# Kernel tuning notes

Hardware: AMD Instinct MI355X
Metric: run time of the kernel (lower is better)

The kernel has to match this reference:

```python
import jax, jax.numpy as jnp
import numpy as np

BS, EMB, RES = 256, 768, 14
N_MASKS, HID, OUT, N_PROJ = 16, 4096, 256, 4
BN_EPS = 1e-5


def setup_inputs() -> dict:
    key = jax.random.key(0)
    ks = jax.random.split(key, 8)
    x = jax.random.normal(ks[0], (BS, EMB, RES, RES), jnp.float32)
    # binary ROI masks over the 14x14 = 196 patch grid
    masks = (jax.random.uniform(ks[1], (BS, N_MASKS, RES * RES)) < 0.3).astype(jnp.float32)
    projection_idx = jax.random.randint(ks[2], (N_MASKS,), 0, N_PROJ, jnp.int32)
    mask_ids = jax.random.randint(ks[3], (BS, N_MASKS), 0, 100, jnp.int32)
    # stacked params for the N_PROJ MLP projectors
    W1 = jax.random.normal(ks[4], (N_PROJ, EMB, HID), jnp.float32) * 0.02
    b1 = jnp.zeros((N_PROJ, HID), jnp.float32)
    gamma = jnp.ones((N_PROJ, HID), jnp.float32)
    beta = jnp.zeros((N_PROJ, HID), jnp.float32)
    W2 = jax.random.normal(ks[5], (N_PROJ, HID, OUT), jnp.float32) * 0.02
    b2 = jnp.zeros((N_PROJ, OUT), jnp.float32)
    return {"x": x, "masks": masks, "projection_idx": projection_idx,
            "mask_ids": mask_ids, "W1": W1, "b1": b1, "gamma": gamma,
            "beta": beta, "W2": W2, "b2": b2}


def reference(x, masks, projection_idx, mask_ids, W1, b1, gamma, beta, W2, b2):
    bs, emb, hx, hy = x.shape
    # [bs, emb, hx, hy] -> [bs, hw, emb]
    emb_local = jnp.transpose(x, (0, 2, 3, 1)).reshape(bs, hx * hy, emb)
    # mask-normalized pooling:  pooled[b,n,:] = mean of embeddings inside mask n
    area = masks.sum(axis=-1, keepdims=True)
    smpl = masks / jnp.maximum(area, 1.0)
    pooled = smpl @ emb_local                       # [bs, n_masks, emb]
    # dense dispatch: run EVERY projector over all pooled tokens (as original)
    h = jnp.einsum('bne,peh->pbnh', pooled, W1) + b1[:, None, None, :]
    # BatchNorm1d in training mode over flattened (bs*n_masks) batch, per projector
    mu = h.mean(axis=(1, 2), keepdims=True)
    var = jnp.mean(jnp.square(h - mu), axis=(1, 2), keepdims=True)  # biased var
    h = (h - mu) * jax.lax.rsqrt(var + BN_EPS) * gamma[:, None, None, :] + beta[:, None, None, :]
    h = jax.nn.relu(h)
    o = jnp.einsum('pbnh,pho->pbno', h, W2) + b2[:, None, None, :]   # [P, bs, n, out]
    # keep only projector projection_idx[n] for mask-slot n (disjoint selection)
    n_proj = W1.shape[0]
    sel = (projection_idx[None, :] == jnp.arange(n_proj)[:, None]).astype(o.dtype)  # [P, n]
    xs = (o * sel[:, None, :, None]).sum(axis=0)     # [bs, n_masks, out]
    return (xs, mask_ids)
```

## Files before the change

kernel.cpp:

```cpp
#include <hip/hip_runtime.h>
#include <hip/hip_bf16.h>

#define BS 256
#define EMB 768
#define HW 196
#define NMASK 16
#define HID 4096
#define OUT 256
#define NPROJ 4
#define MROWS 4096

typedef __attribute__((ext_vector_type(8))) short bf16x8;
typedef __attribute__((ext_vector_type(4))) float f32x4;
typedef __attribute__((ext_vector_type(8))) unsigned short u16x8;

__device__ inline float bf2f(unsigned short u) {
    unsigned int x = ((unsigned int)u) << 16;
    return __builtin_bit_cast(float, x);
}
__device__ inline short f2bfs(float f) {
    return __builtin_bit_cast(short, __float2bfloat16(f));
}

#define GL16(gptr, lptr)                                                     \
    __builtin_amdgcn_global_load_lds(                                        \
        (const __attribute__((address_space(1))) void*)(gptr),               \
        (__attribute__((address_space(3))) void*)(lptr), 16, 0, 0)

__global__ __launch_bounds__(256) void pool_pipe(
    const float* __restrict__ x, const float* __restrict__ masks,
    __hip_bfloat16* __restrict__ pooledG, float* __restrict__ mpB)
{
    __shared__ __align__(16) float xs[37632];
    __shared__ __align__(16) short afr[7 * 64 * 8];
    __shared__ float inv[NMASK];
    const int b = blockIdx.x;
    const int tid = threadIdx.x, lane = tid & 63, w = tid >> 6;
    const int lc = lane & 15, l4 = lane >> 4;
    const float* mb = masks + (size_t)b * NMASK * HW;

    auto STAGE = [&](int s, int c) {
        const char* gsrc = (const char*)(x + ((size_t)b * EMB + w * 192 + c * 16) * HW);
        char* ldst = (char*)xs + w * 37632 + s * 12544;
        #pragma unroll
        for (int i = 0; i < 12; ++i)
            GL16(gsrc + i * 1024 + (size_t)lane * 16, ldst + i * 1024);
        if (lane < 16)
            GL16(gsrc + 12288 + (size_t)lane * 16, ldst + 12288);
    };

    STAGE(0, 0);
    STAGE(1, 1);

    for (int s = tid; s < 7 * 64; s += 256) {
        int m = s & 15, kb = ((s >> 4) & 3) * 8 + (s >> 6) * 32;
        short v[8];
        #pragma unroll
        for (int j = 0; j < 8; ++j) {
            int kk = kb + j;
            v[j] = (kk < HW) ? f2bfs(mb[m * HW + kk]) : (short)0;
        }
        #pragma unroll
        for (int j = 0; j < 8; ++j) afr[s * 8 + j] = v[j];
    }
    if (tid >= 192) {
        int l = tid - 192, m = l >> 2, q = l & 3;
        float a = 0.f;
        for (int hw = q; hw < HW; hw += 4) a += mb[m * HW + hw];
        a += __shfl_xor(a, 1);
        a += __shfl_xor(a, 2);
        if (q == 0) inv[m] = 1.0f / fmaxf(a, 1.0f);
    }
    __syncthreads();

    const bf16x8* afv = (const bf16x8*)afr;

    for (int c = 0; c < 12; ++c) {
        if (c + 2 < 12) STAGE((c + 2) % 3, c + 2);
        if (c < 10)       asm volatile("s_waitcnt vmcnt(26)" ::: "memory");
        else if (c == 10) asm volatile("s_waitcnt vmcnt(13)" ::: "memory");
        else              asm volatile("s_waitcnt vmcnt(0)" ::: "memory");

        const float* xw = (const float*)((const char*)xs + w * 37632 + (c % 3) * 12544);
        f32x4 acc = {};
        #pragma unroll
        for (int kc = 0; kc < 6; ++kc) {
            bf16x8 af = afv[kc * 64 + lane];
            const float* xr = xw + (size_t)lc * 196 + kc * 32 + l4 * 8;
            float4 u0 = *(const float4*)(xr);
            float4 u1 = *(const float4*)(xr + 4);
            bf16x8 bf;
            bf[0] = f2bfs(u0.x); bf[1] = f2bfs(u0.y);
            bf[2] = f2bfs(u0.z); bf[3] = f2bfs(u0.w);
            bf[4] = f2bfs(u1.x); bf[5] = f2bfs(u1.y);
            bf[6] = f2bfs(u1.z); bf[7] = f2bfs(u1.w);
            acc = __builtin_amdgcn_mfma_f32_16x16x32_bf16(af, bf, acc, 0, 0, 0);
        }
        {
            bf16x8 af = afv[6 * 64 + lane];
            bf16x8 bf = {};
            if (l4 == 0) {
                float4 u0 = *(const float4*)(xw + (size_t)lc * 196 + 192);
                bf[0] = f2bfs(u0.x); bf[1] = f2bfs(u0.y);
                bf[2] = f2bfs(u0.z); bf[3] = f2bfs(u0.w);
            }
            acc = __builtin_amdgcn_mfma_f32_16x16x32_bf16(af, bf, acc, 0, 0, 0);
        }

        int e = w * 192 + c * 16 + lc;
        float msum = 0.f;
        #pragma unroll
        for (int j = 0; j < 4; ++j) {
            int m = l4 * 4 + j;
            float v = acc[j] * inv[m];
            msum += v;
            pooledG[((size_t)m * 256 + b) * EMB + e] = __float2bfloat16(v);
        }
        msum += __shfl_xor(msum, 16);
        msum += __shfl_xor(msum, 32);
        if (l4 == 0) mpB[(size_t)b * EMB + e] = msum;
    }
}

__global__ __launch_bounds__(256) void prep(
    const float* __restrict__ W1, const float* __restrict__ W2,
    const __hip_bfloat16* __restrict__ pg,
    __hip_bfloat16* __restrict__ W1T, __hip_bfloat16* __restrict__ W2T,
    __hip_bfloat16* __restrict__ pgT)
{
    __shared__ __align__(16) char sm[64 * 65 * 4];
    const int bid = blockIdx.x, tid = threadIdx.x;
    if (bid < 4096) {
        const float* src; __hip_bfloat16* dst; int R, C, x, y, z;
        if (bid < 3072) { z = bid / 768; int r = bid % 768; x = r % 64; y = r / 64;
                          src = W1; dst = W1T; R = EMB; C = HID; }
        else            { int b2 = bid - 3072; z = b2 / 256; int r = b2 % 256;
                          x = r % 4; y = r / 4; src = W2; dst = W2T; R = HID; C = OUT; }
        float (*tile)[65] = (float(*)[65])sm;
        const float* s = src + (size_t)z * R * C;
        __hip_bfloat16* d = dst + (size_t)z * R * C;
        const int c0 = x * 64, r0 = y * 64;
        for (int i = tid; i < 4096; i += 256) {
            int r = i >> 6, c = i & 63;
            tile[r][c] = s[(size_t)(r0 + r) * C + c0 + c];
        }
        __syncthreads();
        for (int i = tid; i < 4096; i += 256) {
            int c = i >> 6, r = i & 63;
            d[(size_t)(c0 + c) * R + r0 + r] = __float2bfloat16(tile[r][c]);
        }
    } else {
        const int b3 = bid - 4096;
        const int x = b3 % 12, y = b3 / 12;
        __hip_bfloat16 (*tile)[65] = (__hip_bfloat16(*)[65])sm;
        const int c0 = x * 64, r0 = y * 64;
        for (int i = tid; i < 4096; i += 256) {
            int r = i >> 6, c = i & 63;
            tile[r][c] = pg[(size_t)(r0 + r) * EMB + c0 + c];
        }
        __syncthreads();
        for (int i = tid; i < 4096; i += 256) {
            int c = i >> 6, r = i & 63;
            pgT[(size_t)(c0 + c) * MROWS + r0 + r] = tile[r][c];
        }
    }
}

__global__ __launch_bounds__(256) void cgemm(
    const __hip_bfloat16* __restrict__ PT, float* __restrict__ Cpart)
{
    __shared__ __align__(16) __hip_bfloat16 As[128 * 32];
    __shared__ __align__(16) __hip_bfloat16 Bs[128 * 32];
    const int tid = threadIdx.x, lane = tid & 63, wid = tid >> 6;
    const int n0 = blockIdx.x * 128, m0 = blockIdx.y * 128, kbase = blockIdx.z * 512;
    float* Cp = Cpart + (size_t)blockIdx.z * EMB * EMB;
    const int wr = wid >> 1, wc = wid & 1;
    const int l4 = lane >> 4, lc = lane & 15;

    f32x4 acc[4][4] = {};
    for (int k0 = kbase; k0 < kbase + 512; k0 += 32) {
        __syncthreads();
        #pragma unroll
        for (int r = 0; r < 2; ++r) {
            int t = r * 256 + tid;
            int row = t >> 2, ko = (t & 3) * 8;
            GL16(PT + (size_t)(m0 + row) * MROWS + k0 + ko, &As[(r * 256 + wid * 64) * 8]);
        }
        #pragma unroll
        for (int r = 0; r < 2; ++r) {
            int t = r * 256 + tid;
            int row = t >> 2, ko = (t & 3) * 8;
            GL16(PT + (size_t)(n0 + row) * MROWS + k0 + ko, &Bs[(r * 256 + wid * 64) * 8]);
        }
        __syncthreads();
        const bf16x8* Av = (const bf16x8*)As;
        const bf16x8* Bv = (const bf16x8*)Bs;
        bf16x8 a[4], b[4];
        #pragma unroll
        for (int m = 0; m < 4; ++m) a[m] = Av[(wr * 64 + m * 16 + lc) * 4 + l4];
        #pragma unroll
        for (int n = 0; n < 4; ++n) b[n] = Bv[(wc * 64 + n * 16 + lc) * 4 + l4];
        #pragma unroll
        for (int m = 0; m < 4; ++m)
            #pragma unroll
            for (int n = 0; n < 4; ++n)
                acc[m][n] = __builtin_amdgcn_mfma_f32_16x16x32_bf16(a[m], b[n], acc[m][n], 0, 0, 0);
    }
    #pragma unroll
    for (int m = 0; m < 4; ++m)
        #pragma unroll
        for (int n = 0; n < 4; ++n)
            #pragma unroll
            for (int j = 0; j < 4; ++j) {
                int row = m0 + wr * 64 + m * 16 + l4 * 4 + j;
                int col = n0 + wc * 64 + n * 16 + lc;
                Cp[(size_t)row * EMB + col] = acc[m][n][j];
            }
}

__global__ __launch_bounds__(256) void cvt_c(
    const float* __restrict__ Cpart, const float* __restrict__ mpB,
    __hip_bfloat16* __restrict__ Cbf, float* __restrict__ mp)
{
    const int bid = blockIdx.x, tid = threadIdx.x;
    if (bid < 576) {
        int i = (bid * 256 + tid) * 4;
        float sx = 0.f, sy = 0.f, sz = 0.f, sw = 0.f;
        #pragma unroll
        for (int kz = 0; kz < 8; ++kz) {
            float4 v = *(const float4*)(Cpart + (size_t)kz * EMB * EMB + i);
            sx += v.x; sy += v.y; sz += v.z; sw += v.w;
        }
        const float s = 1.0f / 4096.0f;
        Cbf[i + 0] = __float2bfloat16(sx * s);
        Cbf[i + 1] = __float2bfloat16(sy * s);
        Cbf[i + 2] = __float2bfloat16(sz * s);
        Cbf[i + 3] = __float2bfloat16(sw * s);
    } else {
        int e = (bid - 576) * 256 + tid;
        float s = 0.f;
        for (int b = 0; b < 256; ++b) s += mpB[(size_t)b * EMB + e];
        mp[e] = s * (1.0f / 4096.0f);
    }
}

__global__ __launch_bounds__(256) void ugemm(
    const __hip_bfloat16* __restrict__ W1T, const __hip_bfloat16* __restrict__ Cbf,
    const float* __restrict__ mp,
    float* __restrict__ Eh2p, float* __restrict__ Mup)
{
    __shared__ __align__(16) __hip_bfloat16 As[128 * 32];
    __shared__ __align__(16) __hip_bfloat16 Bs[128 * 32];
    const int tid = threadIdx.x, lane = tid & 63, wid = tid >> 6;
    const int n0 = blockIdx.x * 128, m0 = blockIdx.y * 128, p = blockIdx.z;
    const __hip_bfloat16* Ap = W1T + (size_t)p * HID * EMB;
    const int wr = wid >> 1, wc = wid & 1;
    const int l4 = lane >> 4, lc = lane & 15;

    f32x4 acc[4][4] = {};
    for (int k0 = 0; k0 < EMB; k0 += 32) {
        __syncthreads();
        #pragma unroll
        for (int r = 0; r < 2; ++r) {
            int t = r * 256 + tid;
            int row = t >> 2, ko = (t & 3) * 8;
            GL16(Ap + (size_t)(m0 + row) * EMB + k0 + ko, &As[(r * 256 + wid * 64) * 8]);
        }
        #pragma unroll
        for (int r = 0; r < 2; ++r) {
            int t = r * 256 + tid;
            int row = t >> 2, ko = (t & 3) * 8;
            GL16(Cbf + (size_t)(n0 + row) * EMB + k0 + ko, &Bs[(r * 256 + wid * 64) * 8]);
        }
        __syncthreads();
        const bf16x8* Av = (const bf16x8*)As;
        const bf16x8* Bv = (const bf16x8*)Bs;
        bf16x8 a[4], b[4];
        #pragma unroll
        for (int m = 0; m < 4; ++m) a[m] = Av[(wr * 64 + m * 16 + lc) * 4 + l4];
        #pragma unroll
        for (int n = 0; n < 4; ++n) b[n] = Bv[(wc * 64 + n * 16 + lc) * 4 + l4];
        #pragma unroll
        for (int m = 0; m < 4; ++m)
            #pragma unroll
            for (int n = 0; n < 4; ++n)
                acc[m][n] = __builtin_amdgcn_mfma_f32_16x16x32_bf16(a[m], b[n], acc[m][n], 0, 0, 0);
    }

    float mpv[4];
    #pragma unroll
    for (int n = 0; n < 4; ++n) mpv[n] = mp[n0 + wc * 64 + n * 16 + lc];
    #pragma unroll
    for (int m = 0; m < 4; ++m) {
        #pragma unroll
        for (int j = 0; j < 4; ++j) {
            int row = m0 + wr * 64 + m * 16 + l4 * 4 + j;
            const __hip_bfloat16* wrow = Ap + (size_t)row * EMB;
            float e2 = 0.f, mu = 0.f;
            #pragma unroll
            for (int n = 0; n < 4; ++n) {
                int col = n0 + wc * 64 + n * 16 + lc;
                float wv = bf2f(__builtin_bit_cast(unsigned short, wrow[col]));
                e2 += acc[m][n][j] * wv;
                mu += mpv[n] * wv;
            }
            e2 += __shfl_xor(e2, 1); e2 += __shfl_xor(e2, 2);
            e2 += __shfl_xor(e2, 4); e2 += __shfl_xor(e2, 8);
            mu += __shfl_xor(mu, 1); mu += __shfl_xor(mu, 2);
            mu += __shfl_xor(mu, 4); mu += __shfl_xor(mu, 8);
            if (lc == 0) {
                size_t idx = (((size_t)blockIdx.x * 2 + wc) * NPROJ + p) * HID + row;
                Eh2p[idx] = e2;
                Mup [idx] = mu;
            }
        }
    }
}

__global__ __launch_bounds__(512, 2) void gemm1_sel(
    const __hip_bfloat16* __restrict__ A, const __hip_bfloat16* __restrict__ W1T,
    const int* __restrict__ proj,
    const float* __restrict__ Eh2p, const float* __restrict__ Mup,
    const float* __restrict__ gamma, const float* __restrict__ beta,
    __hip_bfloat16* __restrict__ hrelu)
{
    __shared__ __align__(16) short LS[3 * 16384];
    __shared__ float sS[256], sT[256];
    const int tid = threadIdx.x, lane = tid & 63, w = tid >> 6;
    const int wr = w >> 2, wc = w & 3;
    const int lc = lane & 15, l4 = lane >> 4;
    const int n0 = blockIdx.x * 256, m0 = blockIdx.y * 256;
    const int p = proj[blockIdx.y];
    const __hip_bfloat16* Ag = A;
    const __hip_bfloat16* Bg = W1T + (size_t)p * HID * EMB;
    const bf16x8* LSv = (const bf16x8*)LS;

    if (tid < 256) {
        int col = n0 + tid;
        float e2 = 0.f, mu = 0.f;
        #pragma unroll
        for (int s = 0; s < 12; ++s) {
            e2 += Eh2p[((size_t)s * NPROJ + p) * HID + col];
            mu += Mup [((size_t)s * NPROJ + p) * HID + col];
        }
        float var = e2 - mu * mu;
        float is  = rsqrtf(fmaxf(var, 0.0f) + 1e-5f);
        float sc  = gamma[p * HID + col] * is;
        sS[tid] = sc;
        sT[tid] = beta[p * HID + col] - mu * sc;
    }

    auto STAGE = [&](int t) {
        const int sb = (t % 3) * 32768;
        #pragma unroll
        for (int ab = 0; ab < 2; ++ab) {
            const __hip_bfloat16* g = ab ? Bg : Ag;
            const int rbase = ab ? n0 : m0;
            #pragma unroll
            for (int i = 0; i < 2; ++i) {
                int c = (w * 2 + i) * 64 + lane;
                int row = c >> 2, ps = c & 3;
                int ls = ps ^ (row & 3);
                const __hip_bfloat16* src =
                    g + (size_t)(rbase + row) * EMB + t * 32 + ls * 8;
                GL16(src, (char*)LS + sb + ab * 16384 + (w * 2 + i) * 1024);
            }
        }
    };

    f32x4 acc[8][4] = {};

    STAGE(0);
    STAGE(1);
    asm volatile("s_waitcnt vmcnt(4)" ::: "memory");
    __builtin_amdgcn_s_barrier();

    for (int t = 0; t < 24; ++t) {
        if (t + 2 < 24) STAGE(t + 2);
        const int vb = (t % 3) * 2048;

        bf16x8 bfr[4];
        #pragma unroll
        for (int nf = 0; nf < 4; ++nf) {
            int rb = wc * 64 + nf * 16 + lc;
            bfr[nf] = LSv[vb + 1024 + rb * 4 + (l4 ^ (rb & 3))];
        }
        #pragma unroll
        for (int q = 0; q < 4; ++q) {
            bf16x8 afr[2];
            #pragma unroll
            for (int m2 = 0; m2 < 2; ++m2) {
                int ra = wr * 128 + (q * 2 + m2) * 16 + lc;
                afr[m2] = LSv[vb + ra * 4 + (l4 ^ (ra & 3))];
            }
            __builtin_amdgcn_s_setprio(1);
            #pragma unroll
            for (int m2 = 0; m2 < 2; ++m2)
                #pragma unroll
                for (int nf = 0; nf < 4; ++nf)
                    acc[q * 2 + m2][nf] = __builtin_amdgcn_mfma_f32_16x16x32_bf16(
                        afr[m2], bfr[nf], acc[q * 2 + m2][nf], 0, 0, 0);
            __builtin_amdgcn_s_setprio(0);
        }

        if (t + 2 < 24) {
            asm volatile("s_waitcnt vmcnt(4)" ::: "memory");
            __builtin_amdgcn_s_barrier();
        } else if (t + 2 == 24) {
            asm volatile("s_waitcnt vmcnt(0)" ::: "memory");
            __builtin_amdgcn_s_barrier();
        }
    }

    #pragma unroll
    for (int nf = 0; nf < 4; ++nf) {
        int cl = wc * 64 + nf * 16 + lc;
        int col = n0 + cl;
        float s = sS[cl];
        float tt = sT[cl];
        #pragma unroll
        for (int mf = 0; mf < 8; ++mf)
            #pragma unroll
            for (int j = 0; j < 4; ++j) {
                int row = m0 + wr * 128 + mf * 16 + l4 * 4 + j;
                float v = fmaxf(acc[mf][nf][j] * s + tt, 0.0f);
                hrelu[(size_t)row * HID + col] = __float2bfloat16(v);
            }
    }
}

__global__ __launch_bounds__(256) void gemm2(
    const __hip_bfloat16* __restrict__ Hn, const __hip_bfloat16* __restrict__ W2T,
    const int* __restrict__ proj, float* __restrict__ Opart)
{
    __shared__ __align__(16) __hip_bfloat16 As[128 * 32];
    __shared__ __align__(16) __hip_bfloat16 Bs[128 * 32];
    const int tid = threadIdx.x, lane = tid & 63, wid = tid >> 6;
    const int nmask = blockIdx.x;
    const int bc    = blockIdx.y;
    const int ct    = blockIdx.z >> 2, kz = blockIdx.z & 3;
    const int p = proj[nmask];
    const __hip_bfloat16* Ap = Hn + (size_t)(nmask * 256 + bc * 128) * HID;
    const __hip_bfloat16* Bp = W2T + ((size_t)p * OUT + ct * 128) * HID;
    float* Op = Opart + (size_t)kz * MROWS * OUT;
    const int wr = wid >> 1, wc = wid & 1;
    const int l4 = lane >> 4, lc = lane & 15;

    f32x4 acc[4][4] = {};
    for (int k0 = kz * 1024; k0 < kz * 1024 + 1024; k0 += 32) {
        __syncthreads();
        #pragma unroll
        for (int r = 0; r < 2; ++r) {
            int t = r * 256 + tid;
            int row = t >> 2, ko = (t & 3) * 8;
            GL16(Ap + (size_t)row * HID + k0 + ko, &As[(r * 256 + wid * 64) * 8]);
        }
        #pragma unroll
        for (int r = 0; r < 2; ++r) {
            int t = r * 256 + tid;
            int row = t >> 2, ko = (t & 3) * 8;
            GL16(Bp + (size_t)row * HID + k0 + ko, &Bs[(r * 256 + wid * 64) * 8]);
        }
        __syncthreads();
        const bf16x8* Av = (const bf16x8*)As;
        const bf16x8* Bv = (const bf16x8*)Bs;
        bf16x8 a[4], b[4];
        #pragma unroll
        for (int m = 0; m < 4; ++m) a[m] = Av[(wr * 64 + m * 16 + lc) * 4 + l4];
        #pragma unroll
        for (int n = 0; n < 4; ++n) b[n] = Bv[(wc * 64 + n * 16 + lc) * 4 + l4];
        #pragma unroll
        for (int m = 0; m < 4; ++m)
            #pragma unroll
            for (int n = 0; n < 4; ++n)
                acc[m][n] = __builtin_amdgcn_mfma_f32_16x16x32_bf16(a[m], b[n], acc[m][n], 0, 0, 0);
    }

    #pragma unroll
    for (int m = 0; m < 4; ++m)
        #pragma unroll
        for (int n = 0; n < 4; ++n)
            #pragma unroll
            for (int j = 0; j < 4; ++j) {
                int bb = bc * 128 + wr * 64 + m * 16 + l4 * 4 + j;
                int oc = ct * 128 + wc * 64 + n * 16 + lc;
                Op[((size_t)bb * NMASK + nmask) * OUT + oc] = acc[m][n][j];
            }
}

__global__ __launch_bounds__(256) void reduce_out(
    const float* __restrict__ Opart, const float* __restrict__ b2,
    const int* __restrict__ proj, const int* __restrict__ mids,
    float* __restrict__ out)
{
    int i = (blockIdx.x * 256 + threadIdx.x) * 4;
    float sx = 0.f, sy = 0.f, sz = 0.f, sw = 0.f;
    #pragma unroll
    for (int kz = 0; kz < 4; ++kz) {
        float4 v = *(const float4*)(Opart + (size_t)kz * MROWS * OUT + i);
        sx += v.x; sy += v.y; sz += v.z; sw += v.w;
    }
    int nm = (i >> 8) & 15;
    int p  = proj[nm];
    float4 bv = *(const float4*)(b2 + p * OUT + (i & 255));
    float4 r;
    r.x = sx + bv.x; r.y = sy + bv.y; r.z = sz + bv.z; r.w = sw + bv.w;
    *(float4*)(out + i) = r;
    if (blockIdx.x < 16) {
        int t = blockIdx.x * 256 + threadIdx.x;
        out[(size_t)MROWS * OUT + t] = (float)mids[t];
    }
}

extern "C" void kernel_launch(void* const* d_in, const int* in_sizes, int n_in,
                              void* d_out, int out_size, void* d_ws, size_t ws_size,
                              hipStream_t stream)
{
    const float* x     = (const float*)d_in[0];
    const float* masks = (const float*)d_in[1];
    const int*   proj  = (const int*)d_in[2];
    const int*   mids  = (const int*)d_in[3];
    const float* W1    = (const float*)d_in[4];
    const float* gamma = (const float*)d_in[6];
    const float* beta  = (const float*)d_in[7];
    const float* W2    = (const float*)d_in[8];
    const float* b2    = (const float*)d_in[9];
    float* out = (float*)d_out;

    char* ws = (char*)d_ws;
    __hip_bfloat16* pooledG = (__hip_bfloat16*)(ws);
    __hip_bfloat16* W1T     = (__hip_bfloat16*)(ws + 6291456);
    __hip_bfloat16* W2T     = (__hip_bfloat16*)(ws + 31457280);
    float*          mp      = (float*)(ws + 39845888);
    float*          Eh2p    = (float*)(ws + 39848960);
    float*          Mup     = (float*)(ws + 40635392);
    float*          mpB     = (float*)(ws + 41421824);
    char* R = ws + 42208256;
    __hip_bfloat16* pooledT = (__hip_bfloat16*)(R);
    float*          Cpart   = (float*)(R + 6291456);
    __hip_bfloat16* Cbf     = (__hip_bfloat16*)(R + 25165824);
    __hip_bfloat16* hrelu   = (__hip_bfloat16*)(R);
    float*          Opart   = (float*)(R + 33554432);

    pool_pipe<<<256, 256, 0, stream>>>(x, masks, pooledG, mpB);
    prep<<<4864, 256, 0, stream>>>(W1, W2, pooledG, W1T, W2T, pooledT);
    cgemm<<<dim3(6, 6, 8), 256, 0, stream>>>(pooledT, Cpart);
    cvt_c<<<579, 256, 0, stream>>>(Cpart, mpB, Cbf, mp);
    ugemm<<<dim3(6, 32, 4), 256, 0, stream>>>(W1T, Cbf, mp, Eh2p, Mup);
    gemm1_sel<<<dim3(HID / 256, MROWS / 256), 512, 0, stream>>>(pooledG, W1T, proj, Eh2p, Mup, gamma, beta, hrelu);
    gemm2<<<dim3(NMASK, 2, 8), 256, 0, stream>>>(hrelu, W2T, proj, Opart);
    reduce_out<<<(MROWS * OUT) / 1024, 256, 0, stream>>>(Opart, b2, proj, mids, out);
}
```

Baseline: 206.2 us.

## Split pooling kernel across embedding chunks with direct register loads

The pooling kernel goes from one block per batch item, which streamed 768 embedding rows through a triple-buffered LDS pipeline, to 3072 blocks that each handle 64 embedding columns. Each block loads its x rows straight into registers and runs a single MFMA accumulation pass. The aim is to fill the GPU with more blocks and drop the large LDS footprint and waitcnt pipelining. In exchange, every block rebuilds the mask fragments and inverse areas, so that mask work is repeated 12 times per batch item, and the x reads are no longer staged through LDS.

```diff
diff --git a/kernel.cpp b/kernel.cpp
--- a/kernel.cpp
+++ b/kernel.cpp
@@ -27,30 +27,28 @@
         (const __attribute__((address_space(1))) void*)(gptr),               \
         (__attribute__((address_space(3))) void*)(lptr), 16, 0, 0)
 
-__global__ __launch_bounds__(256) void pool_pipe(
+__global__ __launch_bounds__(256) void pool3(
     const float* __restrict__ x, const float* __restrict__ masks,
     __hip_bfloat16* __restrict__ pooledG, float* __restrict__ mpB)
 {
-    __shared__ __align__(16) float xs[37632];
     __shared__ __align__(16) short afr[7 * 64 * 8];
     __shared__ float inv[NMASK];
-    const int b = blockIdx.x;
+    const int bid = blockIdx.x;
+    const int b = bid / 12, ec = bid % 12;
     const int tid = threadIdx.x, lane = tid & 63, w = tid >> 6;
     const int lc = lane & 15, l4 = lane >> 4;
     const float* mb = masks + (size_t)b * NMASK * HW;
 
-    auto STAGE = [&](int s, int c) {
-        const char* gsrc = (const char*)(x + ((size_t)b * EMB + w * 192 + c * 16) * HW);
-        char* ldst = (char*)xs + w * 37632 + s * 12544;
-        #pragma unroll
-        for (int i = 0; i < 12; ++i)
-            GL16(gsrc + i * 1024 + (size_t)lane * 16, ldst + i * 1024);
-        if (lane < 16)
-            GL16(gsrc + 12288 + (size_t)lane * 16, ldst + 12288);
-    };
-
-    STAGE(0, 0);
-    STAGE(1, 1);
+    const int e = ec * 64 + w * 16 + lc;
+    const float* xrow = x + ((size_t)b * EMB + e) * HW;
+    float4 u[6][2];
+    #pragma unroll
+    for (int kc = 0; kc < 6; ++kc) {
+        u[kc][0] = *(const float4*)(xrow + kc * 32 + l4 * 8);
+        u[kc][1] = *(const float4*)(xrow + kc * 32 + l4 * 8 + 4);
+    }
+    float4 ut = (l4 == 0) ? *(const float4*)(xrow + 192)
+                          : float4{0.f, 0.f, 0.f, 0.f};
 
     for (int s = tid; s < 7 * 64; s += 256) {
         int m = s & 15, kb = ((s >> 4) & 3) * 8 + (s >> 6) * 32;
@@ -74,52 +72,38 @@
     __syncthreads();
 
     const bf16x8* afv = (const bf16x8*)afr;
-
-    for (int c = 0; c < 12; ++c) {
-        if (c + 2 < 12) STAGE((c + 2) % 3, c + 2);
-        if (c < 10)       asm volatile("s_waitcnt vmcnt(26)" ::: "memory");
-        else if (c == 10) asm volatile("s_waitcnt vmcnt(13)" ::: "memory");
-        else              asm volatile("s_waitcnt vmcnt(0)" ::: "memory");
-
-        const float* xw = (const float*)((const char*)xs + w * 37632 + (c % 3) * 12544);
-        f32x4 acc = {};
-        #pragma unroll
-        for (int kc = 0; kc < 6; ++kc) {
-            bf16x8 af = afv[kc * 64 + lane];
-            const float* xr = xw + (size_t)lc * 196 + kc * 32 + l4 * 8;
-            float4 u0 = *(const float4*)(xr);
-            float4 u1 = *(const float4*)(xr + 4);
-            bf16x8 bf;
-            bf[0] = f2bfs(u0.x); bf[1] = f2bfs(u0.y);
-            bf[2] = f2bfs(u0.z); bf[3] = f2bfs(u0.w);
-            bf[4] = f2bfs(u1.x); bf[5] = f2bfs(u1.y);
-            bf[6] = f2bfs(u1.z); bf[7] = f2bfs(u1.w);
-            acc = __builtin_amdgcn_mfma_f32_16x16x32_bf16(af, bf, acc, 0, 0, 0);
-        }
-        {
-            bf16x8 af = afv[6 * 64 + lane];
-            bf16x8 bf = {};
-            if (l4 == 0) {
-                float4 u0 = *(const float4*)(xw + (size_t)lc * 196 + 192);
-                bf[0] = f2bfs(u0.x); bf[1] = f2bfs(u0.y);
-                bf[2] = f2bfs(u0.z); bf[3] = f2bfs(u0.w);
-            }
-            acc = __builtin_amdgcn_mfma_f32_16x16x32_bf16(af, bf, acc, 0, 0, 0);
-        }
-
-        int e = w * 192 + c * 16 + lc;
-        float msum = 0.f;
-        #pragma unroll
-        for (int j = 0; j < 4; ++j) {
-            int m = l4 * 4 + j;
-            float v = acc[j] * inv[m];
-            msum += v;
-            pooledG[((size_t)m * 256 + b) * EMB + e] = __float2bfloat16(v);
-        }
-        msum += __shfl_xor(msum, 16);
-        msum += __shfl_xor(msum, 32);
-        if (l4 == 0) mpB[(size_t)b * EMB + e] = msum;
-    }
+    f32x4 acc = {};
+    #pragma unroll
+    for (int kc = 0; kc < 6; ++kc) {
+        bf16x8 af = afv[kc * 64 + lane];
+        bf16x8 bf;
+        bf[0] = f2bfs(u[kc][0].x); bf[1] = f2bfs(u[kc][0].y);
+        bf[2] = f2bfs(u[kc][0].z); bf[3] = f2bfs(u[kc][0].w);
+        bf[4] = f2bfs(u[kc][1].x); bf[5] = f2bfs(u[kc][1].y);
+        bf[6] = f2bfs(u[kc][1].z); bf[7] = f2bfs(u[kc][1].w);
+        acc = __builtin_amdgcn_mfma_f32_16x16x32_bf16(af, bf, acc, 0, 0, 0);
+    }
+    {
+        bf16x8 af = afv[6 * 64 + lane];
+        bf16x8 bf = {};
+        if (l4 == 0) {
+            bf[0] = f2bfs(ut.x); bf[1] = f2bfs(ut.y);
+            bf[2] = f2bfs(ut.z); bf[3] = f2bfs(ut.w);
+        }
+        acc = __builtin_amdgcn_mfma_f32_16x16x32_bf16(af, bf, acc, 0, 0, 0);
+    }
+
+    float msum = 0.f;
+    #pragma unroll
+    for (int j = 0; j < 4; ++j) {
+        int m = l4 * 4 + j;
+        float v = acc[j] * inv[m];
+        msum += v;
+        pooledG[((size_t)m * 256 + b) * EMB + e] = __float2bfloat16(v);
+    }
+    msum += __shfl_xor(msum, 16);
+    msum += __shfl_xor(msum, 32);
+    if (l4 == 0) mpB[(size_t)b * EMB + e] = msum;
 }
 
 __global__ __launch_bounds__(256) void prep(
@@ -542,7 +526,7 @@
     __hip_bfloat16* hrelu   = (__hip_bfloat16*)(R);
     float*          Opart   = (float*)(R + 33554432);
 
-    pool_pipe<<<256, 256, 0, stream>>>(x, masks, pooledG, mpB);
+    pool3<<<3072, 256, 0, stream>>>(x, masks, pooledG, mpB);
     prep<<<4864, 256, 0, stream>>>(W1, W2, pooledG, W1T, W2T, pooledT);
     cgemm<<<dim3(6, 6, 8), 256, 0, stream>>>(pooledT, Cpart);
     cvt_c<<<579, 256, 0, stream>>>(Cpart, mpB, Cbf, mp);
```

After: 221.6 us. 7.5% more time.
